# Performance work log

Hardware: AMD Instinct MI355X
Metric: run time of the kernel (lower is better)

The kernel has to match this reference:

```python
import jax, jax.numpy as jnp
import numpy as np

N_NODES = 100000
N_EDGES = 1600000
IN_DIM = 128
HIDDEN = 128


def setup_inputs() -> dict:
    key = jax.random.key(0)
    k1, k2, k3 = jax.random.split(key, 3)
    x = jax.random.normal(k1, (N_NODES, IN_DIM), dtype=jnp.float32)
    edge_index = jax.random.randint(k2, (2, N_EDGES), 0, N_NODES, dtype=jnp.int64)
    # Glorot-ish init for the GCN weight
    W = jax.random.normal(k3, (IN_DIM, HIDDEN), dtype=jnp.float32) * (1.0 / np.sqrt(IN_DIM))
    b = jnp.zeros((HIDDEN,), dtype=jnp.float32)
    return {"x": x, "edge_index": edge_index, "W": W, "b": b}


def reference(x, edge_index, W, b):
    N = x.shape[0]
    # PyG GCNConv: add self-loops, symmetric deg^{-1/2} normalization,
    # linear transform, scatter-add aggregation at destination, + bias.
    loop = jnp.arange(N, dtype=edge_index.dtype)
    src = jnp.concatenate([edge_index[0], loop])
    dst = jnp.concatenate([edge_index[1], loop])

    ones = jnp.ones(src.shape[0], dtype=x.dtype)
    deg = jax.ops.segment_sum(ones, dst, num_segments=N)  # in-degree incl. self-loop
    dinv = jnp.where(deg > 0, jax.lax.rsqrt(deg), 0.0)
    norm = dinv[src] * dinv[dst]  # [E+N]

    xw = x @ W  # [N, H] dense transform first (GCNConv default)
    msgs = xw[src] * norm[:, None]  # gather + scale, [E+N, H]
    out = jax.ops.segment_sum(msgs, dst, num_segments=N) + b  # scatter-add
    return jax.nn.relu(out)
```

## Files before the change

### kernel.cpp

```cpp
#include <hip/hip_runtime.h>
#include <hip/hip_bf16.h>


#define SCAN_BLK 256
#define NP1 128
#define MAXB 1024

typedef short  short8 __attribute__((ext_vector_type(8)));
typedef float  f32x4  __attribute__((ext_vector_type(4)));

__device__ inline unsigned short f2b(float f) {
    unsigned u = __float_as_uint(f);
    return (unsigned short)((u + 0x7fffu + ((u >> 16) & 1u)) >> 16);
}

__device__ inline void acc4(float4& a, unsigned lo, unsigned hi) {
    a.x += __uint_as_float(lo << 16);
    a.y += __uint_as_float(lo & 0xffff0000u);
    a.z += __uint_as_float(hi << 16);
    a.w += __uint_as_float(hi & 0xffff0000u);
}

__global__ __launch_bounds__(256) void k_hist(const int* __restrict__ dst,
                                              int* __restrict__ hist,
                                              const float* __restrict__ W,
                                              unsigned short* __restrict__ Wt,
                                              int E, int B, int chunk) {
    __shared__ int h[MAXB];
    for (int i = threadIdx.x; i < B; i += 256) h[i] = 0;
    __syncthreads();
    int e0 = blockIdx.x * chunk;
    int e1 = min(E, e0 + chunk);
    for (int e = e0 + threadIdx.x; e < e1; e += 256)
        atomicAdd(&h[dst[e] >> 7], 1);
    __syncthreads();
    for (int i = threadIdx.x; i < B; i += 256)
        hist[i * NP1 + blockIdx.x] = h[i];
    if (blockIdx.x < 64) {
        int i = blockIdx.x * 256 + threadIdx.x;
        int k = i >> 7, n = i & 127;
        Wt[n * 128 + k] = f2b(W[k * 128 + n]);
    }
}

__global__ __launch_bounds__(SCAN_BLK) void k_scanA(const int* __restrict__ in,
                                                    int* __restrict__ bsum, int M) {
    __shared__ int s[SCAN_BLK];
    int t = threadIdx.x;
    int i = blockIdx.x * SCAN_BLK + t;
    s[t] = (i < M) ? in[i] : 0;
    __syncthreads();
    for (int off = SCAN_BLK / 2; off > 0; off >>= 1) {
        if (t < off) s[t] += s[t + off];
        __syncthreads();
    }
    if (t == 0) bsum[blockIdx.x] = s[0];
}

__global__ __launch_bounds__(512) void k_scanB(int* __restrict__ bsum, int nb) {
    __shared__ int s[512];
    int t = threadIdx.x;
    int v = (t < nb) ? bsum[t] : 0;
    s[t] = v;
    __syncthreads();
    for (int off = 1; off < 512; off <<= 1) {
        int add = (t >= off) ? s[t - off] : 0;
        __syncthreads();
        s[t] += add;
        __syncthreads();
    }
    if (t < nb) bsum[t] = s[t] - v;
}

__global__ __launch_bounds__(SCAN_BLK) void k_scanC2(int* __restrict__ data,
                                                     const int* __restrict__ bsum,
                                                     int M) {
    __shared__ int s[SCAN_BLK];
    int t = threadIdx.x;
    int i = blockIdx.x * SCAN_BLK + t;
    int v = (i < M) ? data[i] : 0;
    s[t] = v;
    __syncthreads();
    for (int off = 1; off < SCAN_BLK; off <<= 1) {
        int add = (t >= off) ? s[t - off] : 0;
        __syncthreads();
        s[t] += add;
        __syncthreads();
    }
    if (i < M) data[i] = s[t] - v + bsum[blockIdx.x];
}

__global__ __launch_bounds__(256) void k_scatter(const int* __restrict__ src,
                                                 const int* __restrict__ dst,
                                                 const int* __restrict__ hist_s,
                                                 unsigned* __restrict__ bucketed,
                                                 int E, int B, int chunk) {
    __shared__ int cur[MAXB];
    for (int i = threadIdx.x; i < B; i += 256)
        cur[i] = hist_s[i * NP1 + blockIdx.x];
    __syncthreads();
    int e0 = blockIdx.x * chunk;
    int e1 = min(E, e0 + chunk);
    for (int e = e0 + threadIdx.x; e < e1; e += 256) {
        int d = dst[e];
        int p = atomicAdd(&cur[d >> 7], 1);
        bucketed[p] = (unsigned)src[e] | ((unsigned)(d & 127) << 17);
    }
}

__global__ __launch_bounds__(256) void k_csr(const unsigned* __restrict__ bucketed,
                                             const int* __restrict__ hist_s,
                                             int* __restrict__ csr_src,
                                             int* __restrict__ rowptr,
                                             float* __restrict__ dinv_g,
                                             int E, int B, int N) {
    const int b = blockIdx.x;
    const int t = threadIdx.x;
    const int base = hist_s[b * NP1];
    const int endv = (b + 1 < B) ? hist_s[(b + 1) * NP1] : E;
    const int cnt = endv - base;
    const int node0 = b << 7;

    __shared__ int sdeg[128], sscan[128], cur[128];
    if (t < 128) sdeg[t] = 0;
    __syncthreads();
    for (int i = t; i < cnt; i += 256)
        atomicAdd(&sdeg[bucketed[base + i] >> 17], 1);
    __syncthreads();
    if (t < 128) sscan[t] = sdeg[t];
    __syncthreads();
    for (int off = 1; off < 128; off <<= 1) {
        int add = 0;
        if (t < 128 && t >= off) add = sscan[t - off];
        __syncthreads();
        if (t < 128) sscan[t] += add;
        __syncthreads();
    }
    if (t < 128) {
        int rs = sscan[t] - sdeg[t];
        cur[t] = rs;
        int node = node0 + t;
        if (node < N) {
            rowptr[node] = base + rs;
            dinv_g[node] = rsqrtf((float)(sdeg[t] + 1));
        }
    }
    if (b == B - 1 && t == 0) rowptr[N] = E;
    __syncthreads();
    for (int i = t; i < cnt; i += 256) {
        unsigned w = bucketed[base + i];
        int p = atomicAdd(&cur[w >> 17], 1);
        csr_src[base + p] = (int)(w & 0x1FFFFu);
    }
}

__global__ __launch_bounds__(256) void k_gemm(const float* __restrict__ x,
                                              const unsigned short* __restrict__ Wt,
                                              const float* __restrict__ dinv,
                                              unsigned* __restrict__ xs_out, int N) {
    __shared__ short out_lds[4][16][136];
    const int t = threadIdx.x;
    const int wv = t >> 6;
    const int lane = t & 63;
    const int quad = lane >> 4;
    const int lid = lane & 15;
    const int row0 = blockIdx.x * 64;

    int grow = row0 + wv * 16 + lid;
    int growc = grow < N ? grow : N - 1;
    short8 af[4];
#pragma unroll
    for (int q = 0; q < 4; ++q) {
        const float4* xr = (const float4*)(x + (size_t)growc * 128 + q * 32 + quad * 8);
        float4 f0 = xr[0], f1 = xr[1];
        af[q][0] = (short)f2b(f0.x); af[q][1] = (short)f2b(f0.y);
        af[q][2] = (short)f2b(f0.z); af[q][3] = (short)f2b(f0.w);
        af[q][4] = (short)f2b(f1.x); af[q][5] = (short)f2b(f1.y);
        af[q][6] = (short)f2b(f1.z); af[q][7] = (short)f2b(f1.w);
    }

    int drow = row0 + wv * 16 + quad * 4;
    float4 dv4;
    if (drow + 3 < N)      dv4 = *(const float4*)(dinv + drow);
    else {
        dv4.x = dinv[min(drow + 0, N - 1)];
        dv4.y = dinv[min(drow + 1, N - 1)];
        dv4.z = dinv[min(drow + 2, N - 1)];
        dv4.w = dinv[min(drow + 3, N - 1)];
    }

#pragma unroll
    for (int c = 0; c < 8; ++c) {
        f32x4 acc = {0.f, 0.f, 0.f, 0.f};
#pragma unroll
        for (int q = 0; q < 4; ++q) {
            const short8* bp = (const short8*)(Wt + (size_t)(c * 16 + lid) * 128 +
                                               q * 32 + quad * 8);
            acc = __builtin_amdgcn_mfma_f32_16x16x32_bf16(af[q], *bp, acc, 0, 0, 0);
        }
        out_lds[wv][quad * 4 + 0][c * 16 + lid] = (short)f2b(acc[0] * dv4.x);
        out_lds[wv][quad * 4 + 1][c * 16 + lid] = (short)f2b(acc[1] * dv4.y);
        out_lds[wv][quad * 4 + 2][c * 16 + lid] = (short)f2b(acc[2] * dv4.z);
        out_lds[wv][quad * 4 + 3][c * 16 + lid] = (short)f2b(acc[3] * dv4.w);
    }
    __syncthreads();

    int rl = lane >> 2;
    int cseg = lane & 3;
    int grow2 = row0 + wv * 16 + rl;
    if (grow2 < N) {
        uint4* dstp = (uint4*)(xs_out + (size_t)grow2 * 64);
        const uint4* srcp = (const uint4*)((const char*)&out_lds[wv][rl][0] + cseg * 64);
#pragma unroll
        for (int tt = 0; tt < 4; ++tt) dstp[cseg * 4 + tt] = srcp[tt];
    }
}

__global__ __launch_bounds__(256) void k_aggregate(const uint4* __restrict__ xs4,
                                                   const int* __restrict__ csr_src,
                                                   const int* __restrict__ rowptr,
                                                   const float* __restrict__ dinv,
                                                   const float* __restrict__ bias,
                                                   float* __restrict__ out, int N) {
    const int wave = threadIdx.x >> 6;
    const int lane = threadIdx.x & 63;
    const int n = blockIdx.x * 4 + wave;
    if (n >= N) return;
    const int grp = lane >> 4;
    const int sub = lane & 15;

    const int rs = rowptr[n];
    const int c  = rowptr[n + 1] - rs;
    const float dv = dinv[n];

    int idxreg = (lane < c) ? csr_src[rs + lane] : 0;

    float4 a0 = make_float4(0.f, 0.f, 0.f, 0.f);
    float4 a1 = make_float4(0.f, 0.f, 0.f, 0.f);
    const int cmain = c < 64 ? c : 64;

    int i = 0;
    for (; i + 16 <= cmain; i += 16) {
#pragma unroll
        for (int j = 0; j < 4; ++j) {
            int row = __shfl(idxreg, i + 4 * j + grp);
            uint4 u = xs4[(size_t)row * 16 + sub];
            acc4(a0, u.x, u.y);
            acc4(a1, u.z, u.w);
        }
    }
    if (i < cmain) {
#pragma unroll
        for (int j = 0; j < 4; ++j) {
            int e = i + 4 * j + grp;
            int row = __shfl(idxreg, e);
            uint4 u = xs4[(size_t)row * 16 + sub];
            if (e >= cmain) { u.x = 0u; u.y = 0u; u.z = 0u; u.w = 0u; }
            acc4(a0, u.x, u.y);
            acc4(a1, u.z, u.w);
        }
    }
    for (int e0 = 64; e0 < c; e0 += 4) {
        int e = e0 + grp;
        uint4 u = make_uint4(0u, 0u, 0u, 0u);
        if (e < c) {
            int row = csr_src[rs + e];
            u = xs4[(size_t)row * 16 + sub];
        }
        acc4(a0, u.x, u.y);
        acc4(a1, u.z, u.w);
    }

    a0.x += __shfl_xor(a0.x, 16); a0.x += __shfl_xor(a0.x, 32);
    a0.y += __shfl_xor(a0.y, 16); a0.y += __shfl_xor(a0.y, 32);
    a0.z += __shfl_xor(a0.z, 16); a0.z += __shfl_xor(a0.z, 32);
    a0.w += __shfl_xor(a0.w, 16); a0.w += __shfl_xor(a0.w, 32);
    a1.x += __shfl_xor(a1.x, 16); a1.x += __shfl_xor(a1.x, 32);
    a1.y += __shfl_xor(a1.y, 16); a1.y += __shfl_xor(a1.y, 32);
    a1.z += __shfl_xor(a1.z, 16); a1.z += __shfl_xor(a1.z, 32);
    a1.w += __shfl_xor(a1.w, 16); a1.w += __shfl_xor(a1.w, 32);

    if (lane < 32) {
        const uint2* xs2 = (const uint2*)xs4;
        int p = lane >> 4;
        int f4 = (lane & 15) * 2 + p;
        float4 av = p ? a1 : a0;
        uint2 su = xs2[(size_t)n * 32 + f4];
        acc4(av, su.x, su.y);
        float4 bb = ((const float4*)bias)[f4];
        float4 o;
        o.x = fmaxf(dv * av.x + bb.x, 0.f);
        o.y = fmaxf(dv * av.y + bb.y, 0.f);
        o.z = fmaxf(dv * av.z + bb.z, 0.f);
        o.w = fmaxf(dv * av.w + bb.w, 0.f);
        ((float4*)(out + (size_t)n * 128))[f4] = o;
    }
}

extern "C" void kernel_launch(void* const* d_in, const int* in_sizes, int n_in,
                              void* d_out, int out_size, void* d_ws, size_t ws_size,
                              hipStream_t stream) {
    const float* x   = (const float*)d_in[0];
    const int*   ei  = (const int*)d_in[1];
    const float* W   = (const float*)d_in[2];
    const float* b   = (const float*)d_in[3];
    float*       out = (float*)d_out;

    const int N = in_sizes[0] / 128;
    const int E = in_sizes[1] / 2;
    const int* src = ei;
    const int* dst = ei + E;

    const int B = (N + 127) >> 7;
    const int M = B * NP1;
    const int chunk = (E + NP1 - 1) / NP1;

    auto align = [](size_t v) { return (v + 255) & ~(size_t)255; };
    char* p = (char*)d_ws;
    int*            hist     = (int*)p;            p += align((size_t)M * 4);
    int*            bsum     = (int*)p;            p += align(512 * 4);
    int*            rowptr   = (int*)p;            p += align(((size_t)N + 1) * 4);
    float*          dinv     = (float*)p;          p += align((size_t)N * 4);
    unsigned*       bucketed = (unsigned*)p;       p += align((size_t)E * 4);
    int*            csr_src  = (int*)p;            p += align((size_t)E * 4);
    unsigned*       xs       = (unsigned*)p;       p += align((size_t)N * 64 * 4);
    unsigned short* Wt       = (unsigned short*)p; p += align(128 * 128 * 2);
    (void)ws_size;

    const int nbM = (M + SCAN_BLK - 1) / SCAN_BLK;

    k_hist   <<<NP1, 256, 0, stream>>>(dst, hist, W, Wt, E, B, chunk);
    k_scanA  <<<nbM, 256, 0, stream>>>(hist, bsum, M);
    k_scanB  <<<1, 512, 0, stream>>>(bsum, nbM);
    k_scanC2 <<<nbM, 256, 0, stream>>>(hist, bsum, M);
    k_scatter<<<NP1, 256, 0, stream>>>(src, dst, hist, bucketed, E, B, chunk);
    k_csr    <<<B, 256, 0, stream>>>(bucketed, hist, csr_src, rowptr, dinv, E, B, N);
    k_gemm   <<<(N + 63) / 64, 256, 0, stream>>>(x, Wt, dinv, xs, N);
    k_aggregate<<<(N + 3) / 4, 256, 0, stream>>>((const uint4*)xs, csr_src, rowptr,
                                                 dinv, b, out, N);
}
```

Measured before the change: 262.3 us.

## Assign one 16-lane group per node in aggregation with zero sentinel row

The aggregation kernel now gives each node a 16-lane group instead of a full wave, so four nodes share a wave. Each lane loads a 16-byte slice of the bf16 row and there is no cross-group shuffle reduction at the end. A zeroed sentinel row at index N is written by the GEMM so padded edge slots can load it without branching, and addresses are built with shift/or arithmetic. Nontemporal loads of x and stores of out are added to limit cache pollution. The trade-off is more divergence, since nodes with different degrees now share a wave.

```diff
diff --git a/kernel.cpp b/kernel.cpp
--- a/kernel.cpp
+++ b/kernel.cpp
@@ -171,12 +171,13 @@
     short8 af[4];
 #pragma unroll
     for (int q = 0; q < 4; ++q) {
-        const float4* xr = (const float4*)(x + (size_t)growc * 128 + q * 32 + quad * 8);
-        float4 f0 = xr[0], f1 = xr[1];
-        af[q][0] = (short)f2b(f0.x); af[q][1] = (short)f2b(f0.y);
-        af[q][2] = (short)f2b(f0.z); af[q][3] = (short)f2b(f0.w);
-        af[q][4] = (short)f2b(f1.x); af[q][5] = (short)f2b(f1.y);
-        af[q][6] = (short)f2b(f1.z); af[q][7] = (short)f2b(f1.w);
+        const f32x4* xr = (const f32x4*)(x + (size_t)growc * 128 + q * 32 + quad * 8);
+        f32x4 f0 = __builtin_nontemporal_load(xr);
+        f32x4 f1 = __builtin_nontemporal_load(xr + 1);
+        af[q][0] = (short)f2b(f0[0]); af[q][1] = (short)f2b(f0[1]);
+        af[q][2] = (short)f2b(f0[2]); af[q][3] = (short)f2b(f0[3]);
+        af[q][4] = (short)f2b(f1[0]); af[q][5] = (short)f2b(f1[1]);
+        af[q][6] = (short)f2b(f1[2]); af[q][7] = (short)f2b(f1[3]);
     }
 
     int drow = row0 + wv * 16 + quad * 4;
@@ -208,11 +209,17 @@
     int rl = lane >> 2;
     int cseg = lane & 3;
     int grow2 = row0 + wv * 16 + rl;
-    if (grow2 < N) {
+    if (grow2 <= N) {
         uint4* dstp = (uint4*)(xs_out + (size_t)grow2 * 64);
-        const uint4* srcp = (const uint4*)((const char*)&out_lds[wv][rl][0] + cseg * 64);
-#pragma unroll
-        for (int tt = 0; tt < 4; ++tt) dstp[cseg * 4 + tt] = srcp[tt];
+        if (grow2 < N) {
+            const uint4* srcp = (const uint4*)((const char*)&out_lds[wv][rl][0] + cseg * 64);
+#pragma unroll
+            for (int tt = 0; tt < 4; ++tt) dstp[cseg * 4 + tt] = srcp[tt];
+        } else {
+            uint4 z = make_uint4(0u, 0u, 0u, 0u);
+#pragma unroll
+            for (int tt = 0; tt < 4; ++tt) dstp[cseg * 4 + tt] = z;
+        }
     }
 }
 
@@ -222,79 +229,62 @@
                                                    const float* __restrict__ dinv,
                                                    const float* __restrict__ bias,
                                                    float* __restrict__ out, int N) {
-    const int wave = threadIdx.x >> 6;
-    const int lane = threadIdx.x & 63;
-    const int n = blockIdx.x * 4 + wave;
+    const int t = threadIdx.x;
+    const int lane = t & 63;
+    const int sub = lane & 15;
+    const int gbase = lane & 48;
+    const int n = blockIdx.x * 16 + (t >> 4);
     if (n >= N) return;
-    const int grp = lane >> 4;
-    const int sub = lane & 15;
 
     const int rs = rowptr[n];
-    const int c  = rowptr[n + 1] - rs;
+    const int re = rowptr[n + 1];
     const float dv = dinv[n];
-
-    int idxreg = (lane < c) ? csr_src[rs + lane] : 0;
+    const char* xb = (const char*)xs4;
+    const unsigned subo = (unsigned)sub << 4;
 
     float4 a0 = make_float4(0.f, 0.f, 0.f, 0.f);
     float4 a1 = make_float4(0.f, 0.f, 0.f, 0.f);
-    const int cmain = c < 64 ? c : 64;
-
-    int i = 0;
-    for (; i + 16 <= cmain; i += 16) {
-#pragma unroll
-        for (int j = 0; j < 4; ++j) {
-            int row = __shfl(idxreg, i + 4 * j + grp);
-            uint4 u = xs4[(size_t)row * 16 + sub];
-            acc4(a0, u.x, u.y);
-            acc4(a1, u.z, u.w);
+
+    for (int i0 = rs; i0 < re; i0 += 16) {
+        int m = re - i0; if (m > 16) m = 16;
+        int idx = N;
+        if (sub < m) idx = csr_src[i0 + sub];
+        for (int j = 0; j < m; j += 4) {
+            int r0 = __shfl(idx, gbase + j);
+            int r1 = __shfl(idx, gbase + j + 1);
+            int r2 = __shfl(idx, gbase + j + 2);
+            int r3 = __shfl(idx, gbase + j + 3);
+            uint4 u0 = *(const uint4*)(xb + ((((unsigned)r0) << 8) | subo));
+            uint4 u1 = *(const uint4*)(xb + ((((unsigned)r1) << 8) | subo));
+            uint4 u2 = *(const uint4*)(xb + ((((unsigned)r2) << 8) | subo));
+            uint4 u3 = *(const uint4*)(xb + ((((unsigned)r3) << 8) | subo));
+            acc4(a0, u0.x, u0.y); acc4(a1, u0.z, u0.w);
+            acc4(a0, u1.x, u1.y); acc4(a1, u1.z, u1.w);
+            acc4(a0, u2.x, u2.y); acc4(a1, u2.z, u2.w);
+            acc4(a0, u3.x, u3.y); acc4(a1, u3.z, u3.w);
         }
     }
-    if (i < cmain) {
-#pragma unroll
-        for (int j = 0; j < 4; ++j) {
-            int e = i + 4 * j + grp;
-            int row = __shfl(idxreg, e);
-            uint4 u = xs4[(size_t)row * 16 + sub];
-            if (e >= cmain) { u.x = 0u; u.y = 0u; u.z = 0u; u.w = 0u; }
-            acc4(a0, u.x, u.y);
-            acc4(a1, u.z, u.w);
-        }
-    }
-    for (int e0 = 64; e0 < c; e0 += 4) {
-        int e = e0 + grp;
-        uint4 u = make_uint4(0u, 0u, 0u, 0u);
-        if (e < c) {
-            int row = csr_src[rs + e];
-            u = xs4[(size_t)row * 16 + sub];
-        }
-        acc4(a0, u.x, u.y);
-        acc4(a1, u.z, u.w);
-    }
-
-    a0.x += __shfl_xor(a0.x, 16); a0.x += __shfl_xor(a0.x, 32);
-    a0.y += __shfl_xor(a0.y, 16); a0.y += __shfl_xor(a0.y, 32);
-    a0.z += __shfl_xor(a0.z, 16); a0.z += __shfl_xor(a0.z, 32);
-    a0.w += __shfl_xor(a0.w, 16); a0.w += __shfl_xor(a0.w, 32);
-    a1.x += __shfl_xor(a1.x, 16); a1.x += __shfl_xor(a1.x, 32);
-    a1.y += __shfl_xor(a1.y, 16); a1.y += __shfl_xor(a1.y, 32);
-    a1.z += __shfl_xor(a1.z, 16); a1.z += __shfl_xor(a1.z, 32);
-    a1.w += __shfl_xor(a1.w, 16); a1.w += __shfl_xor(a1.w, 32);
-
-    if (lane < 32) {
-        const uint2* xs2 = (const uint2*)xs4;
-        int p = lane >> 4;
-        int f4 = (lane & 15) * 2 + p;
-        float4 av = p ? a1 : a0;
-        uint2 su = xs2[(size_t)n * 32 + f4];
-        acc4(av, su.x, su.y);
-        float4 bb = ((const float4*)bias)[f4];
-        float4 o;
-        o.x = fmaxf(dv * av.x + bb.x, 0.f);
-        o.y = fmaxf(dv * av.y + bb.y, 0.f);
-        o.z = fmaxf(dv * av.z + bb.z, 0.f);
-        o.w = fmaxf(dv * av.w + bb.w, 0.f);
-        ((float4*)(out + (size_t)n * 128))[f4] = o;
-    }
+
+    uint4 su = *(const uint4*)(xb + ((((unsigned)n) << 8) | subo));
+    acc4(a0, su.x, su.y);
+    acc4(a1, su.z, su.w);
+
+    const float4* bp = (const float4*)bias;
+    float4 b0 = bp[sub * 2];
+    float4 b1 = bp[sub * 2 + 1];
+    f32x4 o0, o1;
+    o0[0] = fmaxf(dv * a0.x + b0.x, 0.f);
+    o0[1] = fmaxf(dv * a0.y + b0.y, 0.f);
+    o0[2] = fmaxf(dv * a0.z + b0.z, 0.f);
+    o0[3] = fmaxf(dv * a0.w + b0.w, 0.f);
+    o1[0] = fmaxf(dv * a1.x + b1.x, 0.f);
+    o1[1] = fmaxf(dv * a1.y + b1.y, 0.f);
+    o1[2] = fmaxf(dv * a1.z + b1.z, 0.f);
+    o1[3] = fmaxf(dv * a1.w + b1.w, 0.f);
+
+    f32x4* op = (f32x4*)(out + (size_t)n * 128 + sub * 8);
+    __builtin_nontemporal_store(o0, op);
+    __builtin_nontemporal_store(o1, op + 1);
 }
 
 extern "C" void kernel_launch(void* const* d_in, const int* in_sizes, int n_in,
@@ -323,7 +313,7 @@
     float*          dinv     = (float*)p;          p += align((size_t)N * 4);
     unsigned*       bucketed = (unsigned*)p;       p += align((size_t)E * 4);
     int*            csr_src  = (int*)p;            p += align((size_t)E * 4);
-    unsigned*       xs       = (unsigned*)p;       p += align((size_t)N * 64 * 4);
+    unsigned*       xs       = (unsigned*)p;       p += align(((size_t)N + 1) * 64 * 4);
     unsigned short* Wt       = (unsigned short*)p; p += align(128 * 128 * 2);
     (void)ws_size;
 
@@ -336,6 +326,6 @@
     k_scatter<<<NP1, 256, 0, stream>>>(src, dst, hist, bucketed, E, B, chunk);
     k_csr    <<<B, 256, 0, stream>>>(bucketed, hist, csr_src, rowptr, dinv, E, B, N);
     k_gemm   <<<(N + 63) / 64, 256, 0, stream>>>(x, Wt, dinv, xs, N);
-    k_aggregate<<<(N + 3) / 4, 256, 0, stream>>>((const uint4*)xs, csr_src, rowptr,
-                                                 dinv, b, out, N);
-}
+    k_aggregate<<<(N + 15) / 16, 256, 0, stream>>>((const uint4*)xs, csr_src, rowptr,
+                                                   dinv, b, out, N);
+}
```

New measurement: 282.2 us. +7.6%, slower.
